# Kernel optimization log

Measured on AMD Instinct MI355X. Metric: run time of the kernel, lower is better.

## Reference

```python
import jax, jax.numpy as jnp
import numpy as np
from jax import lax

# Inference-mode (training=False) ROIGenerator constants
PRE_NMS_TOPK = 1000
POST_NMS_TOPK = 1000
IOU_THRESHOLD = 0.7
SCORE_THRESHOLD = 0.0

LEVEL_SIZES = {2: 196608, 3: 49152, 4: 12288, 5: 3072}
BATCH = 8


def _make_boxes(key, shape):
    # valid yxyx boxes: y1 < y2, x1 < x2
    k1, k2 = jax.random.split(key)
    yx = jax.random.uniform(k1, shape[:-1] + (2,), dtype=jnp.float32) * 1000.0
    hw = jax.random.uniform(k2, shape[:-1] + (2,), dtype=jnp.float32) * 100.0 + 1.0
    return jnp.concatenate([yx, yx + hw], axis=-1)  # [B, N, 4] yxyx


def setup_inputs() -> dict:
    key = jax.random.key(0)
    ks = jax.random.split(key, 8)
    inp = {}
    for i, lvl in enumerate(sorted(LEVEL_SIZES)):
        n = LEVEL_SIZES[lvl]
        inp[f"boxes_p{lvl}"] = _make_boxes(ks[2 * i], (BATCH, n, 4))
        inp[f"scores_p{lvl}"] = jax.random.normal(ks[2 * i + 1], (BATCH, n), dtype=jnp.float32)
    return inp


def _pairwise_iou(b):
    # b: [B, K, 4] in yxyx -> iou: [B, K, K]
    y1, x1, y2, x2 = jnp.split(b, 4, axis=-1)           # each [B, K, 1]
    area = ((y2 - y1) * (x2 - x1))[..., 0]              # [B, K]
    iy1 = jnp.maximum(y1, jnp.swapaxes(y1, 1, 2))
    ix1 = jnp.maximum(x1, jnp.swapaxes(x1, 1, 2))
    iy2 = jnp.minimum(y2, jnp.swapaxes(y2, 1, 2))
    ix2 = jnp.minimum(x2, jnp.swapaxes(x2, 1, 2))
    ih = jnp.clip(iy2 - iy1, 0.0)
    iw = jnp.clip(ix2 - ix1, 0.0)
    inter = ih * iw                                     # [B, K, K]
    union = area[:, :, None] + area[:, None, :] - inter
    return jnp.where(union > 0, inter / union, 0.0)


def _per_level_gen(boxes, scores):
    # boxes: [B, N, 4] yxyx, scores: [B, N]
    n = scores.shape[1]
    pre_k = min(n, PRE_NMS_TOPK)
    post_k = min(n, POST_NMS_TOPK)

    s, idx = lax.top_k(scores, pre_k)                    # sorted desc, [B, pre_k]
    b = jnp.take_along_axis(boxes, idx[..., None], axis=1)  # [B, pre_k, 4]

    suppress = _pairwise_iou(b) > IOU_THRESHOLD          # [B, pre_k, pre_k]
    keep0 = s > SCORE_THRESHOLD                          # score filter
    ar = jnp.arange(pre_k)

    def step(i, keep):
        # box i suppressed if any earlier kept box overlaps it
        sup_i = jnp.any(suppress[:, :, i] & keep & (ar < i)[None, :], axis=1)
        return keep.at[:, i].set(keep[:, i] & ~sup_i)

    keep = lax.fori_loop(0, pre_k, step, keep0)          # [B, pre_k]

    # kept indices first (stable -> preserves score order), padded selection
    order = jnp.argsort((~keep).astype(jnp.int32), axis=1)  # jax argsort is stable
    sel = order[:, :post_k]                              # [B, post_k]
    num_valid = keep.sum(axis=1)                         # [B]

    level_rois = jnp.take_along_axis(b, sel[..., None], axis=1)   # [B, post_k, 4]
    level_scores = jnp.take_along_axis(s, sel, axis=1)            # [B, post_k]
    vmask = jnp.arange(post_k)[None, :] < num_valid[:, None]      # zero out padding
    level_rois = level_rois * vmask[..., None].astype(level_rois.dtype)
    level_scores = level_scores * vmask.astype(level_scores.dtype)
    return level_rois, level_scores


def _roi_generator(boxes_p2, boxes_p3, boxes_p4, boxes_p5,
                   scores_p2, scores_p3, scores_p4, scores_p5):
    levels = [(boxes_p2, scores_p2), (boxes_p3, scores_p3),
              (boxes_p4, scores_p4), (boxes_p5, scores_p5)]
    rois, roi_scores = [], []
    for b, s in levels:
        r, rs = _per_level_gen(b, s)
        rois.append(r)
        roi_scores.append(rs)
    rois = jnp.concatenate(rois, axis=1)                 # [B, 4*post_k, 4]
    roi_scores = jnp.concatenate(roi_scores, axis=1)     # [B, 4*post_k]
    overall_k = min(roi_scores.shape[1], POST_NMS_TOPK)
    roi_scores, sorted_idx = lax.top_k(roi_scores, overall_k)
    rois = jnp.take_along_axis(rois, sorted_idx[..., None], axis=1)
    return rois, roi_scores


def reference(boxes_p2, boxes_p3, boxes_p4, boxes_p5,
              scores_p2, scores_p3, scores_p4, scores_p5):
    return _roi_generator(boxes_p2, boxes_p3, boxes_p4, boxes_p5,
                          scores_p2, scores_p3, scores_p4, scores_p5)
```

## Files before the change

kernel.cpp:

```cpp
#include <hip/hip_runtime.h>

#define PRE_K 1000
#define CAP   2048
#define NBIN  8192
#define NB    1000
#define NW    16
#define TOT   4000
#define NLVL  4
#define BATCH 8
#define HB    8
#define MBM   16

__device__ __forceinline__ unsigned f2key(float f) {
    unsigned u = __float_as_uint(f);
    return (u & 0x80000000u) ? ~u : (u | 0x80000000u);
}
__device__ __forceinline__ float key2f(unsigned k) {
    unsigned u = (k & 0x80000000u) ? (k & 0x7FFFFFFFu) : ~k;
    return __uint_as_float(u);
}
__device__ __forceinline__ const float* lvl_scores(
    const float* s0, const float* s1, const float* s2, const float* s3, int lvl) {
    switch (lvl) { case 0: return s0; case 1: return s1; case 2: return s2; default: return s3; }
}
__device__ __forceinline__ const float* lvl_boxes(
    const float* b0, const float* b1, const float* b2, const float* b3, int lvl) {
    switch (lvl) { case 0: return b0; case 1: return b1; case 2: return b2; default: return b3; }
}
__device__ __forceinline__ int lvl_n(int lvl) {
    const int sizes[4] = {196608, 49152, 12288, 3072};
    return sizes[lvl];
}
__device__ __forceinline__ float bcast_f(float v, int i) {
    return __int_as_float(__builtin_amdgcn_readlane(__float_as_int(v), i));
}

__global__ __launch_bounds__(512) void hist_kernel(
    const float* __restrict__ scores0, const float* __restrict__ scores1,
    const float* __restrict__ scores2, const float* __restrict__ scores3,
    unsigned* __restrict__ ghist,
    unsigned* __restrict__ counters,
    unsigned long long* __restrict__ ws_nz)
{
    const int blk = blockIdx.x / HB;
    const int hb  = blockIdx.x % HB;
    const int b   = blk >> 2;
    const int lvl = blk & 3;
    const int n   = lvl_n(lvl);
    const float* sc = lvl_scores(scores0, scores1, scores2, scores3, lvl) + (size_t)b * n;

    __shared__ unsigned lhist[2][NBIN];
    const int tid = threadIdx.x;
    const int rep = (tid >> 6) & 1;
    for (int i = tid; i < 2 * NBIN; i += 512) (&lhist[0][0])[i] = 0u;
    if (hb == 0) {
        if (tid == 0) counters[blk] = 0u;
        if (tid < NW) ws_nz[(size_t)blk * NW + tid] = 0ull;
    }
    __syncthreads();

    const float4* sc4 = (const float4*)sc;
    const int n4 = n >> 2;
    for (int i = hb * 512 + tid; i < n4; i += HB * 512) {
        float4 v = sc4[i];
        atomicAdd(&lhist[rep][f2key(v.x) >> 19], 1u);
        atomicAdd(&lhist[rep][f2key(v.y) >> 19], 1u);
        atomicAdd(&lhist[rep][f2key(v.z) >> 19], 1u);
        atomicAdd(&lhist[rep][f2key(v.w) >> 19], 1u);
    }
    __syncthreads();

    unsigned* gh = ghist + ((size_t)blk * HB + hb) * NBIN;
    for (int i = tid; i < NBIN; i += 512)
        gh[i] = lhist[0][i] + lhist[1][i];
}

__global__ __launch_bounds__(512) void collect_kernel(
    const float* __restrict__ scores0, const float* __restrict__ scores1,
    const float* __restrict__ scores2, const float* __restrict__ scores3,
    const unsigned* __restrict__ ghist,
    unsigned* __restrict__ counters,
    unsigned long long* __restrict__ cand)
{
    const int blk = blockIdx.x / HB;
    const int hb  = blockIdx.x % HB;
    const int b   = blk >> 2;
    const int lvl = blk & 3;
    const int n   = lvl_n(lvl);
    const float* sc = lvl_scores(scores0, scores1, scores2, scores3, lvl) + (size_t)b * n;
    unsigned long long* candp = cand + (size_t)blk * CAP;

    __shared__ unsigned hsum[NBIN];
    __shared__ unsigned csum[256];
    __shared__ int s_chunk;
    __shared__ unsigned s_before, sT;
    __shared__ unsigned long long cbuf[CAP];
    __shared__ unsigned ccnt, cbase;

    const int tid  = threadIdx.x;
    const int lane = tid & 63;
    if (tid == 0) ccnt = 0;

    for (int i = tid; i < NBIN; i += 512) {
        unsigned v = 0;
        #pragma unroll
        for (int p = 0; p < HB; ++p)
            v += ghist[((size_t)blk * HB + p) * NBIN + i];
        hsum[i] = v;
    }
    __syncthreads();
    if (tid < 256) {
        unsigned s = 0;
        #pragma unroll
        for (int k = 0; k < 32; ++k)
            s += hsum[tid * 32 + ((k + tid) & 31)];
        csum[tid] = s;
    }
    __syncthreads();
    if (tid < 256) {
        unsigned suf = 0;
        for (int c = tid + 1; c < 256; ++c) suf += csum[c];
        if (suf < PRE_K && suf + csum[tid] >= PRE_K) { s_chunk = tid; s_before = suf; }
    }
    __syncthreads();
    if (tid == 0) {
        int C = s_chunk;
        unsigned acc = s_before;
        int T = C * 32;
        for (int bin = C * 32 + 31; bin >= C * 32; --bin) {
            acc += hsum[bin];
            if (acc >= PRE_K) { T = bin; break; }
        }
        sT = (unsigned)T;
    }
    __syncthreads();
    const unsigned T = sT;

    for (int i = hb * 512 + tid; i < n; i += HB * 512) {
        unsigned key = f2key(sc[i]);
        bool pred = (key >> 19) >= T;
        unsigned long long act = __ballot(pred);
        if (act) {
            int leader = __ffsll((long long)act) - 1;
            unsigned base = 0;
            if (lane == leader) base = atomicAdd(&ccnt, (unsigned)__popcll(act));
            base = __shfl(base, leader, 64);
            if (pred) {
                unsigned pos = base + (unsigned)__popcll(act & ((1ull << lane) - 1ull));
                if (pos < CAP)
                    cbuf[pos] = ((unsigned long long)key << 32) | (unsigned)(~i);
            }
        }
    }
    __syncthreads();
    unsigned cnt = ccnt; if (cnt > CAP) cnt = CAP;
    if (tid == 0) cbase = atomicAdd(&counters[blk], cnt);
    __syncthreads();
    const unsigned gb = cbase;
    for (unsigned i = tid; i < cnt; i += 512) {
        unsigned p = gb + i;
        if (p < CAP) candp[p] = cbuf[i];
    }
}

__global__ __launch_bounds__(1024) void sortemit_kernel(
    const float* __restrict__ boxes0, const float* __restrict__ boxes1,
    const float* __restrict__ boxes2, const float* __restrict__ boxes3,
    const unsigned* __restrict__ counters,
    const unsigned long long* __restrict__ cand,
    float* __restrict__ ws_scores,
    float* __restrict__ ws_boxes)
{
    const int blk = blockIdx.x;
    const int b   = blk >> 2;
    const int lvl = blk & 3;
    const int n   = lvl_n(lvl);
    const float* bx = lvl_boxes(boxes0, boxes1, boxes2, boxes3, lvl) + (size_t)b * n * 4;
    const unsigned long long* candp = cand + (size_t)blk * CAP;

    __shared__ unsigned long long arr[CAP];
    const int tid = threadIdx.x;
    unsigned cnt = counters[blk]; if (cnt > CAP) cnt = CAP;

    for (int i = tid; i < CAP; i += 1024)
        arr[i] = (i < (int)cnt) ? candp[i] : 0ull;
    __syncthreads();

    for (unsigned kk = 2; kk <= CAP; kk <<= 1) {
        for (unsigned j = kk >> 1; j > 0; j >>= 1) {
            for (unsigned i = tid; i < CAP; i += 1024) {
                unsigned p = i ^ j;
                if (p > i) {
                    unsigned long long a = arr[i], c = arr[p];
                    bool desc = ((i & kk) == 0);
                    if (desc ? (a < c) : (a > c)) { arr[i] = c; arr[p] = a; }
                }
            }
            __syncthreads();
        }
    }

    for (int r = tid; r < PRE_K; r += 1024) {
        unsigned long long c = arr[r];
        unsigned key = (unsigned)(c >> 32);
        int idx = (int)(~(unsigned)c);
        ws_scores[(size_t)blk * PRE_K + r] = key2f(key);
        float* dst = ws_boxes + ((size_t)blk * PRE_K + r) * 4;
        const float* src = bx + (size_t)idx * 4;
        dst[0] = src[0]; dst[1] = src[1]; dst[2] = src[2]; dst[3] = src[3];
    }
}

__global__ __launch_bounds__(256) void mask_kernel(
    const float* __restrict__ ws_boxes,
    unsigned long long* __restrict__ ws_mask,
    unsigned long long* __restrict__ ws_nz)
{
    const int blk  = blockIdx.x / MBM;
    const int mb   = blockIdx.x % MBM;
    const int tid  = threadIdx.x;
    const int lane = tid & 63;
    const int wv   = tid >> 6;

    __shared__ float4 sbox[1024];

    const float4* bxp = (const float4*)(ws_boxes + (size_t)blk * NB * 4);
    for (int i = tid; i < 1024; i += 256)
        sbox[i] = (i < NB) ? bxp[i] : make_float4(0.f, 0.f, 0.f, 0.f);
    __syncthreads();

    unsigned long long* maskp = ws_mask + (size_t)blk * NB * NW;
    unsigned long long* nzp   = ws_nz + (size_t)blk * NW;
    const double CSUM = (double)__uint_as_float(0x3F333333u)
                      + (double)__uint_as_float(0x3F333334u);

    for (int t = mb * 4 + wv; t < 136; t += MBM * 4) {
        int w = 0, acc = 0;
        while (acc + w + 1 <= t) { acc += w + 1; ++w; }
        const int rb = t - acc;
        const int rbase = rb * 64;

        const float4 rbx = sbox[rbase + lane];
        const float   ra = (rbx.z - rbx.x) * (rbx.w - rbx.y);
        const float4 cbx = sbox[w * 64 + lane];
        const float   ca = (cbx.z - cbx.x) * (cbx.w - cbx.y);

        unsigned long long myw = 0ull;
        #pragma unroll
        for (int jj = 0; jj < 64; ++jj) {
            const float cy1 = bcast_f(cbx.x, jj);
            const float cx1 = bcast_f(cbx.y, jj);
            const float cy2 = bcast_f(cbx.z, jj);
            const float cx2 = bcast_f(cbx.w, jj);
            const float caj = bcast_f(ca, jj);
            float iy1 = fmaxf(rbx.x, cy1);
            float ix1 = fmaxf(rbx.y, cx1);
            float iy2 = fminf(rbx.z, cy2);
            float ix2 = fminf(rbx.w, cx2);
            float ih = fmaxf(iy2 - iy1, 0.0f);
            float iw = fmaxf(ix2 - ix1, 0.0f);
            float inter = ih * iw;
            float uni = ra + caj - inter;
            bool pred = (uni > 0.0f) &&
                        (2.0 * (double)inter >= CSUM * (double)uni);
            myw |= ((unsigned long long)pred) << jj;
        }
        if (w == rb)
            myw &= ~((2ull << lane) - 1ull);
        if (rbase + lane < NB)
            maskp[(size_t)(rbase + lane) * NW + w] = myw;
        unsigned long long nzb = __ballot(myw != 0ull);
        if (lane == 0 && nzb) atomicOr(&nzp[rb], nzb);
    }
}

__global__ __launch_bounds__(1024) void greedy_kernel(
    float* __restrict__ ws_scores,
    float* __restrict__ ws_boxes,
    const unsigned long long* __restrict__ ws_mask,
    const unsigned long long* __restrict__ ws_nz)
{
    const int blk  = blockIdx.x;
    const int tid  = threadIdx.x;
    const int lane = tid & 63;
    const int wv   = tid >> 6;

    __shared__ unsigned long long Mrow[NB * NW];
    __shared__ float4 sbox[NB];
    __shared__ float  ssc[NB];
    __shared__ unsigned long long nzlds[NW];
    __shared__ unsigned long long keepw[NW];
    __shared__ int wprefix[NW];
    __shared__ int slist[NB];
    __shared__ int sL;

    float* scp = ws_scores + (size_t)blk * NB;
    float* bxp = ws_boxes  + (size_t)blk * NB * 4;
    const unsigned long long* mrows = ws_mask + (size_t)blk * NB * NW;

    if (tid < NW) nzlds[tid] = ws_nz[(size_t)blk * NW + tid];
    for (int i = tid; i < NB; i += 1024) {
        sbox[i] = ((const float4*)bxp)[i];
        ssc[i]  = scp[i];
    }
    {
        const int j = wv * 64 + lane;
        bool pred = (j < NB) && (scp[j] > 0.0f);
        unsigned long long bal = __ballot(pred);
        if (lane == 0) keepw[wv] = bal;
    }
    __syncthreads();

    if (tid == 0) {
        int L = 0;
        for (int c = 0; c < NW; ++c) {
            unsigned long long p = nzlds[c];
            while (p) {
                int i = __ffsll((long long)p) - 1;
                slist[L++] = c * 64 + i;
                p &= p - 1;
            }
        }
        sL = L;
    }
    __syncthreads();
    const int L = sL;

    for (int idx = tid; idx < L * NW; idx += 1024) {
        int r = slist[idx >> 4];
        Mrow[idx] = mrows[(size_t)r * NW + (idx & 15)];
    }
    __syncthreads();

    if (tid < 64) {
        unsigned long long kp = (lane < NW) ? keepw[lane] : 0ull;
        unsigned long long mnext = (L > 0 && lane < NW) ? Mrow[lane] : 0ull;
        int rnext = (L > 0) ? slist[0] : 0;
        for (int k = 0; k < L; ++k) {
            unsigned long long m = mnext;
            const int r = rnext;
            if (k + 1 < L) {
                rnext = slist[k + 1];
                mnext = (lane < NW) ? Mrow[(size_t)(k + 1) * NW + lane] : 0ull;
            }
            const int c = r >> 6;
            unsigned klo = (unsigned)__builtin_amdgcn_readlane((int)(unsigned)kp, c);
            unsigned khi = (unsigned)__builtin_amdgcn_readlane((int)(unsigned)(kp >> 32), c);
            unsigned long long kw = ((unsigned long long)khi << 32) | klo;
            if ((kw >> (r & 63)) & 1ull) {
                unsigned long long mm = (lane >= c) ? m : 0ull;
                kp &= ~mm;
            }
        }
        if (lane < NW) keepw[lane] = kp;
    }
    __syncthreads();
    if (tid == 0) {
        int acc = 0;
        for (int w = 0; w < NW; ++w) { wprefix[w] = acc; acc += __popcll(keepw[w]); }
    }
    __syncthreads();

    for (int i = tid; i < NB; i += 1024) scp[i] = 0.0f;
    for (int i = tid; i < NB * 4; i += 1024) bxp[i] = 0.0f;
    __syncthreads();
    for (int i = tid; i < NB; i += 1024) {
        const int w = i >> 6;
        const unsigned long long kw = keepw[w];
        if ((kw >> (i & 63)) & 1ull) {
            int rank = wprefix[w] + __popcll(kw & ((1ull << (i & 63)) - 1ull));
            scp[rank] = ssc[i];
            float4 bb = sbox[i];
            float* dst = bxp + (size_t)rank * 4;
            dst[0] = bb.x; dst[1] = bb.y; dst[2] = bb.z; dst[3] = bb.w;
        }
    }
}

__global__ __launch_bounds__(1024) void final_merge_kernel(
    const float* __restrict__ ws_scores,
    const float* __restrict__ ws_boxes,
    float* __restrict__ out)
{
    const int blk = blockIdx.x;
    const int b   = blk >> 2;
    const int lvl = blk & 3;
    const int tid = threadIdx.x;

    __shared__ unsigned long long lists[NLVL][PRE_K];

    for (int i = tid; i < TOT; i += 1024) {
        unsigned u = f2key(ws_scores[(size_t)b * TOT + i]);
        lists[i / PRE_K][i % PRE_K] =
            ((unsigned long long)u << 32) | (unsigned)(~i);
    }
    __syncthreads();

    float* out_rois   = out;
    float* out_scores = out + 32000;

    for (int r = tid; r < PRE_K; r += 1024) {
        const unsigned long long c = lists[lvl][r];
        int rank = r;
        #pragma unroll
        for (int l = 0; l < NLVL; ++l) {
            if (l == lvl) continue;
            int lo = 0, hi = PRE_K;
            while (lo < hi) {
                int mid = (lo + hi) >> 1;
                if (lists[l][mid] > c) lo = mid + 1; else hi = mid;
            }
            rank += lo;
        }
        if (rank < PRE_K) {
            out_scores[(size_t)b * PRE_K + rank] = key2f((unsigned)(c >> 32));
            const int pos = lvl * PRE_K + r;
            const float4 bb = ((const float4*)ws_boxes)[(size_t)b * TOT + pos];
            float* dst = out_rois + ((size_t)b * PRE_K + rank) * 4;
            dst[0] = bb.x; dst[1] = bb.y; dst[2] = bb.z; dst[3] = bb.w;
        }
    }
}

extern "C" void kernel_launch(void* const* d_in, const int* in_sizes, int n_in,
                              void* d_out, int out_size, void* d_ws, size_t ws_size,
                              hipStream_t stream) {
    const float* boxes0  = (const float*)d_in[0];
    const float* scores0 = (const float*)d_in[1];
    const float* boxes1  = (const float*)d_in[2];
    const float* scores1 = (const float*)d_in[3];
    const float* boxes2  = (const float*)d_in[4];
    const float* scores2 = (const float*)d_in[5];
    const float* boxes3  = (const float*)d_in[6];
    const float* scores3 = (const float*)d_in[7];
    float* out = (float*)d_out;

    char* base = (char*)d_ws;
    float* ws_scores = (float*)base;
    float* ws_boxes  = (float*)(base + 128000);
    unsigned long long* ws_mask = (unsigned long long*)(base + 640000);
    unsigned long long* ws_nz   = (unsigned long long*)(base + 4736000);
    unsigned long long* cand    = (unsigned long long*)(base + 4740096);
    unsigned* ghist             = (unsigned*)(base + 5264384);
    unsigned* counters          = (unsigned*)(base + 13652992);

    hist_kernel<<<BATCH * NLVL * HB, 512, 0, stream>>>(
        scores0, scores1, scores2, scores3, ghist, counters, ws_nz);
    collect_kernel<<<BATCH * NLVL * HB, 512, 0, stream>>>(
        scores0, scores1, scores2, scores3, ghist, counters, cand);
    sortemit_kernel<<<BATCH * NLVL, 1024, 0, stream>>>(
        boxes0, boxes1, boxes2, boxes3, counters, cand, ws_scores, ws_boxes);
    mask_kernel<<<BATCH * NLVL * MBM, 256, 0, stream>>>(ws_boxes, ws_mask, ws_nz);
    greedy_kernel<<<BATCH * NLVL, 1024, 0, stream>>>(ws_scores, ws_boxes, ws_mask, ws_nz);
    final_merge_kernel<<<BATCH * NLVL, 1024, 0, stream>>>(ws_scores, ws_boxes, out);
}
```

Before: 114.6 us.

## Fuse histogram, collect, sort, mask and greedy NMS into one per-level kernel

Replaces five kernels (histogram, candidate collect, bitonic sort, IoU mask, greedy NMS) with one kernel per (batch, level) block of 1024 threads. A single shared buffer is reused for the 4-replica histogram, the candidate list and the XOR-swizzled IoU mask, so the mask and candidates never go through global memory. This removes launch overhead and global round-trips. In exchange the histogram and collect passes now run on only 32 blocks instead of 256, which lowers parallelism for the large P2 level (196k scores read twice by one block).

```diff
diff --git a/kernel.cpp b/kernel.cpp
--- a/kernel.cpp
+++ b/kernel.cpp
@@ -3,13 +3,12 @@
 #define PRE_K 1000
 #define CAP   2048
 #define NBIN  8192
+#define NREP  4
 #define NB    1000
 #define NW    16
 #define TOT   4000
 #define NLVL  4
 #define BATCH 8
-#define HB    8
-#define MBM   16
 
 __device__ __forceinline__ unsigned f2key(float f) {
     unsigned u = __float_as_uint(f);
@@ -35,139 +34,11 @@
     return __int_as_float(__builtin_amdgcn_readlane(__float_as_int(v), i));
 }
 
-__global__ __launch_bounds__(512) void hist_kernel(
-    const float* __restrict__ scores0, const float* __restrict__ scores1,
-    const float* __restrict__ scores2, const float* __restrict__ scores3,
-    unsigned* __restrict__ ghist,
-    unsigned* __restrict__ counters,
-    unsigned long long* __restrict__ ws_nz)
-{
-    const int blk = blockIdx.x / HB;
-    const int hb  = blockIdx.x % HB;
-    const int b   = blk >> 2;
-    const int lvl = blk & 3;
-    const int n   = lvl_n(lvl);
-    const float* sc = lvl_scores(scores0, scores1, scores2, scores3, lvl) + (size_t)b * n;
-
-    __shared__ unsigned lhist[2][NBIN];
-    const int tid = threadIdx.x;
-    const int rep = (tid >> 6) & 1;
-    for (int i = tid; i < 2 * NBIN; i += 512) (&lhist[0][0])[i] = 0u;
-    if (hb == 0) {
-        if (tid == 0) counters[blk] = 0u;
-        if (tid < NW) ws_nz[(size_t)blk * NW + tid] = 0ull;
-    }
-    __syncthreads();
-
-    const float4* sc4 = (const float4*)sc;
-    const int n4 = n >> 2;
-    for (int i = hb * 512 + tid; i < n4; i += HB * 512) {
-        float4 v = sc4[i];
-        atomicAdd(&lhist[rep][f2key(v.x) >> 19], 1u);
-        atomicAdd(&lhist[rep][f2key(v.y) >> 19], 1u);
-        atomicAdd(&lhist[rep][f2key(v.z) >> 19], 1u);
-        atomicAdd(&lhist[rep][f2key(v.w) >> 19], 1u);
-    }
-    __syncthreads();
-
-    unsigned* gh = ghist + ((size_t)blk * HB + hb) * NBIN;
-    for (int i = tid; i < NBIN; i += 512)
-        gh[i] = lhist[0][i] + lhist[1][i];
-}
-
-__global__ __launch_bounds__(512) void collect_kernel(
-    const float* __restrict__ scores0, const float* __restrict__ scores1,
-    const float* __restrict__ scores2, const float* __restrict__ scores3,
-    const unsigned* __restrict__ ghist,
-    unsigned* __restrict__ counters,
-    unsigned long long* __restrict__ cand)
-{
-    const int blk = blockIdx.x / HB;
-    const int hb  = blockIdx.x % HB;
-    const int b   = blk >> 2;
-    const int lvl = blk & 3;
-    const int n   = lvl_n(lvl);
-    const float* sc = lvl_scores(scores0, scores1, scores2, scores3, lvl) + (size_t)b * n;
-    unsigned long long* candp = cand + (size_t)blk * CAP;
-
-    __shared__ unsigned hsum[NBIN];
-    __shared__ unsigned csum[256];
-    __shared__ int s_chunk;
-    __shared__ unsigned s_before, sT;
-    __shared__ unsigned long long cbuf[CAP];
-    __shared__ unsigned ccnt, cbase;
-
-    const int tid  = threadIdx.x;
-    const int lane = tid & 63;
-    if (tid == 0) ccnt = 0;
-
-    for (int i = tid; i < NBIN; i += 512) {
-        unsigned v = 0;
-        #pragma unroll
-        for (int p = 0; p < HB; ++p)
-            v += ghist[((size_t)blk * HB + p) * NBIN + i];
-        hsum[i] = v;
-    }
-    __syncthreads();
-    if (tid < 256) {
-        unsigned s = 0;
-        #pragma unroll
-        for (int k = 0; k < 32; ++k)
-            s += hsum[tid * 32 + ((k + tid) & 31)];
-        csum[tid] = s;
-    }
-    __syncthreads();
-    if (tid < 256) {
-        unsigned suf = 0;
-        for (int c = tid + 1; c < 256; ++c) suf += csum[c];
-        if (suf < PRE_K && suf + csum[tid] >= PRE_K) { s_chunk = tid; s_before = suf; }
-    }
-    __syncthreads();
-    if (tid == 0) {
-        int C = s_chunk;
-        unsigned acc = s_before;
-        int T = C * 32;
-        for (int bin = C * 32 + 31; bin >= C * 32; --bin) {
-            acc += hsum[bin];
-            if (acc >= PRE_K) { T = bin; break; }
-        }
-        sT = (unsigned)T;
-    }
-    __syncthreads();
-    const unsigned T = sT;
-
-    for (int i = hb * 512 + tid; i < n; i += HB * 512) {
-        unsigned key = f2key(sc[i]);
-        bool pred = (key >> 19) >= T;
-        unsigned long long act = __ballot(pred);
-        if (act) {
-            int leader = __ffsll((long long)act) - 1;
-            unsigned base = 0;
-            if (lane == leader) base = atomicAdd(&ccnt, (unsigned)__popcll(act));
-            base = __shfl(base, leader, 64);
-            if (pred) {
-                unsigned pos = base + (unsigned)__popcll(act & ((1ull << lane) - 1ull));
-                if (pos < CAP)
-                    cbuf[pos] = ((unsigned long long)key << 32) | (unsigned)(~i);
-            }
-        }
-    }
-    __syncthreads();
-    unsigned cnt = ccnt; if (cnt > CAP) cnt = CAP;
-    if (tid == 0) cbase = atomicAdd(&counters[blk], cnt);
-    __syncthreads();
-    const unsigned gb = cbase;
-    for (unsigned i = tid; i < cnt; i += 512) {
-        unsigned p = gb + i;
-        if (p < CAP) candp[p] = cbuf[i];
-    }
-}
-
-__global__ __launch_bounds__(1024) void sortemit_kernel(
-    const float* __restrict__ boxes0, const float* __restrict__ boxes1,
-    const float* __restrict__ boxes2, const float* __restrict__ boxes3,
-    const unsigned* __restrict__ counters,
-    const unsigned long long* __restrict__ cand,
+__global__ __launch_bounds__(1024) void fused_level_kernel(
+    const float* __restrict__ boxes0, const float* __restrict__ scores0,
+    const float* __restrict__ boxes1, const float* __restrict__ scores1,
+    const float* __restrict__ boxes2, const float* __restrict__ scores2,
+    const float* __restrict__ boxes3, const float* __restrict__ scores3,
     float* __restrict__ ws_scores,
     float* __restrict__ ws_boxes)
 {
@@ -175,15 +46,105 @@
     const int b   = blk >> 2;
     const int lvl = blk & 3;
     const int n   = lvl_n(lvl);
+    const float* sc = lvl_scores(scores0, scores1, scores2, scores3, lvl) + (size_t)b * n;
     const float* bx = lvl_boxes(boxes0, boxes1, boxes2, boxes3, lvl) + (size_t)b * n * 4;
-    const unsigned long long* candp = cand + (size_t)blk * CAP;
-
-    __shared__ unsigned long long arr[CAP];
-    const int tid = threadIdx.x;
-    unsigned cnt = counters[blk]; if (cnt > CAP) cnt = CAP;
-
-    for (int i = tid; i < CAP; i += 1024)
-        arr[i] = (i < (int)cnt) ? candp[i] : 0ull;
+
+    __shared__ __align__(16) unsigned long long A[1024 * NW];
+    __shared__ float4 sbox[1024];
+    __shared__ float  ssc[1024];
+    __shared__ int    slist[NB];
+    __shared__ unsigned csum[256];
+    __shared__ unsigned long long nzlds[NW], keepw[NW];
+    __shared__ int wprefix[NW];
+    __shared__ unsigned s_chunk, s_before, sT, ccnt;
+    __shared__ int sL;
+
+    const int tid  = threadIdx.x;
+    const int lane = tid & 63;
+    const int wv   = tid >> 6;
+
+    unsigned* lhist = (unsigned*)A;
+    for (int i = tid; i < NREP * NBIN; i += 1024) lhist[i] = 0u;
+    if (tid < NW) nzlds[tid] = 0ull;
+    if (tid == 0) ccnt = 0u;
+    __syncthreads();
+    {
+        const unsigned roff = (unsigned)(wv & (NREP - 1)) * NBIN;
+        const float4* sc4 = (const float4*)sc;
+        const int n4 = n >> 2;
+        for (int i = tid; i < n4; i += 1024) {
+            float4 v = sc4[i];
+            atomicAdd(&lhist[roff + (f2key(v.x) >> 19)], 1u);
+            atomicAdd(&lhist[roff + (f2key(v.y) >> 19)], 1u);
+            atomicAdd(&lhist[roff + (f2key(v.z) >> 19)], 1u);
+            atomicAdd(&lhist[roff + (f2key(v.w) >> 19)], 1u);
+        }
+    }
+    __syncthreads();
+
+    if (tid < 256) {
+        unsigned s = 0;
+        #pragma unroll 8
+        for (int k = 0; k < 32; ++k) {
+            int bin = tid * 32 + ((k + tid) & 31);
+            s += lhist[bin] + lhist[NBIN + bin] + lhist[2*NBIN + bin] + lhist[3*NBIN + bin];
+        }
+        csum[tid] = s;
+    }
+    __syncthreads();
+    if (tid < 256) {
+        unsigned suf = 0;
+        for (int c = tid + 1; c < 256; ++c) suf += csum[c];
+        if (suf < PRE_K && suf + csum[tid] >= PRE_K) { s_chunk = tid; s_before = suf; }
+    }
+    __syncthreads();
+    if (tid == 0) {
+        int C = (int)s_chunk;
+        unsigned acc = s_before;
+        int T = C * 32;
+        for (int bin = C * 32 + 31; bin >= C * 32; --bin) {
+            acc += lhist[bin] + lhist[NBIN + bin] + lhist[2*NBIN + bin] + lhist[3*NBIN + bin];
+            if (acc >= PRE_K) { T = bin; break; }
+        }
+        sT = (unsigned)T;
+    }
+    __syncthreads();
+    const unsigned T = sT;
+    __syncthreads();
+
+    unsigned long long* cbuf = A;
+    {
+        const float4* sc4 = (const float4*)sc;
+        const int n4 = n >> 2;
+        for (int i = tid; i < n4; i += 1024) {
+            float4 v = sc4[i];
+            #pragma unroll
+            for (int c4 = 0; c4 < 4; ++c4) {
+                float f = (c4 == 0) ? v.x : (c4 == 1) ? v.y : (c4 == 2) ? v.z : v.w;
+                unsigned key = f2key(f);
+                bool pred = (key >> 19) >= T;
+                unsigned long long act = __ballot(pred);
+                if (act) {
+                    int leader = __ffsll((long long)act) - 1;
+                    unsigned base = 0;
+                    if (lane == leader) base = atomicAdd(&ccnt, (unsigned)__popcll(act));
+                    base = __shfl(base, leader, 64);
+                    if (pred) {
+                        unsigned pos = base + (unsigned)__popcll(act & ((1ull << lane) - 1ull));
+                        int idx = i * 4 + c4;
+                        if (pos < CAP)
+                            cbuf[pos] = ((unsigned long long)key << 32) | (unsigned)(~idx);
+                    }
+                }
+            }
+        }
+    }
+    __syncthreads();
+    {
+        unsigned cnt = ccnt; if (cnt > CAP) cnt = CAP;
+        for (int i = tid; i < CAP; i += 1024)
+            if (i >= (int)cnt) cbuf[i] = 0ull;
+    }
     __syncthreads();
 
     for (unsigned kk = 2; kk <= CAP; kk <<= 1) {
@@ -191,50 +152,31 @@
             for (unsigned i = tid; i < CAP; i += 1024) {
                 unsigned p = i ^ j;
                 if (p > i) {
-                    unsigned long long a = arr[i], c = arr[p];
+                    unsigned long long a = cbuf[i], c = cbuf[p];
                     bool desc = ((i & kk) == 0);
-                    if (desc ? (a < c) : (a > c)) { arr[i] = c; arr[p] = a; }
+                    if (desc ? (a < c) : (a > c)) { cbuf[i] = c; cbuf[p] = a; }
                 }
             }
             __syncthreads();
         }
     }
 
-    for (int r = tid; r < PRE_K; r += 1024) {
-        unsigned long long c = arr[r];
-        unsigned key = (unsigned)(c >> 32);
-        int idx = (int)(~(unsigned)c);
-        ws_scores[(size_t)blk * PRE_K + r] = key2f(key);
-        float* dst = ws_boxes + ((size_t)blk * PRE_K + r) * 4;
-        const float* src = bx + (size_t)idx * 4;
-        dst[0] = src[0]; dst[1] = src[1]; dst[2] = src[2]; dst[3] = src[3];
-    }
-}
-
-__global__ __launch_bounds__(256) void mask_kernel(
-    const float* __restrict__ ws_boxes,
-    unsigned long long* __restrict__ ws_mask,
-    unsigned long long* __restrict__ ws_nz)
-{
-    const int blk  = blockIdx.x / MBM;
-    const int mb   = blockIdx.x % MBM;
-    const int tid  = threadIdx.x;
-    const int lane = tid & 63;
-    const int wv   = tid >> 6;
-
-    __shared__ float4 sbox[1024];
-
-    const float4* bxp = (const float4*)(ws_boxes + (size_t)blk * NB * 4);
-    for (int i = tid; i < 1024; i += 256)
-        sbox[i] = (i < NB) ? bxp[i] : make_float4(0.f, 0.f, 0.f, 0.f);
-    __syncthreads();
-
-    unsigned long long* maskp = ws_mask + (size_t)blk * NB * NW;
-    unsigned long long* nzp   = ws_nz + (size_t)blk * NW;
-    const double CSUM = (double)__uint_as_float(0x3F333333u)
-                      + (double)__uint_as_float(0x3F333334u);
-
-    for (int t = mb * 4 + wv; t < 136; t += MBM * 4) {
+    {
+        const int r = tid;
+        if (r < PRE_K) {
+            unsigned long long c = cbuf[r];
+            int idx = (int)(~(unsigned)c);
+            sbox[r] = ((const float4*)bx)[idx];
+            ssc[r]  = key2f((unsigned)(c >> 32));
+        } else {
+            sbox[r] = make_float4(0.f, 0.f, 0.f, 0.f);
+            ssc[r]  = 0.f;
+        }
+    }
+    __syncthreads();
+
+    unsigned long long* Mlds = A;
+    for (int t = wv; t < 136; t += 16) {
         int w = 0, acc = 0;
         while (acc + w + 1 <= t) { acc += w + 1; ++w; }
         const int rb = t - acc;
@@ -244,6 +186,8 @@
         const float   ra = (rbx.z - rbx.x) * (rbx.w - rbx.y);
         const float4 cbx = sbox[w * 64 + lane];
         const float   ca = (cbx.z - cbx.x) * (cbx.w - cbx.y);
+        const double CSUM = (double)__uint_as_float(0x3F333333u)
+                          + (double)__uint_as_float(0x3F333334u);
 
         unsigned long long myw = 0ull;
         #pragma unroll
@@ -267,45 +211,14 @@
         }
         if (w == rb)
             myw &= ~((2ull << lane) - 1ull);
-        if (rbase + lane < NB)
-            maskp[(size_t)(rbase + lane) * NW + w] = myw;
+        const int row = rbase + lane;
+        Mlds[row * NW + (w ^ (lane & 15))] = myw;
         unsigned long long nzb = __ballot(myw != 0ull);
-        if (lane == 0 && nzb) atomicOr(&nzp[rb], nzb);
-    }
-}
-
-__global__ __launch_bounds__(1024) void greedy_kernel(
-    float* __restrict__ ws_scores,
-    float* __restrict__ ws_boxes,
-    const unsigned long long* __restrict__ ws_mask,
-    const unsigned long long* __restrict__ ws_nz)
-{
-    const int blk  = blockIdx.x;
-    const int tid  = threadIdx.x;
-    const int lane = tid & 63;
-    const int wv   = tid >> 6;
-
-    __shared__ unsigned long long Mrow[NB * NW];
-    __shared__ float4 sbox[NB];
-    __shared__ float  ssc[NB];
-    __shared__ unsigned long long nzlds[NW];
-    __shared__ unsigned long long keepw[NW];
-    __shared__ int wprefix[NW];
-    __shared__ int slist[NB];
-    __shared__ int sL;
-
-    float* scp = ws_scores + (size_t)blk * NB;
-    float* bxp = ws_boxes  + (size_t)blk * NB * 4;
-    const unsigned long long* mrows = ws_mask + (size_t)blk * NB * NW;
-
-    if (tid < NW) nzlds[tid] = ws_nz[(size_t)blk * NW + tid];
-    for (int i = tid; i < NB; i += 1024) {
-        sbox[i] = ((const float4*)bxp)[i];
-        ssc[i]  = scp[i];
+        if (lane == 0 && nzb) atomicOr(&nzlds[rb], nzb);
     }
     {
         const int j = wv * 64 + lane;
-        bool pred = (j < NB) && (scp[j] > 0.0f);
+        bool pred = (j < NB) && (ssc[j] > 0.0f);
         unsigned long long bal = __ballot(pred);
         if (lane == 0) keepw[wv] = bal;
     }
@@ -325,23 +238,17 @@
     }
     __syncthreads();
     const int L = sL;
-
-    for (int idx = tid; idx < L * NW; idx += 1024) {
-        int r = slist[idx >> 4];
-        Mrow[idx] = mrows[(size_t)r * NW + (idx & 15)];
-    }
-    __syncthreads();
-
     if (tid < 64) {
         unsigned long long kp = (lane < NW) ? keepw[lane] : 0ull;
-        unsigned long long mnext = (L > 0 && lane < NW) ? Mrow[lane] : 0ull;
         int rnext = (L > 0) ? slist[0] : 0;
+        unsigned long long mnext = (L > 0 && lane < NW)
+            ? Mlds[rnext * NW + (lane ^ (rnext & 15))] : 0ull;
         for (int k = 0; k < L; ++k) {
             unsigned long long m = mnext;
             const int r = rnext;
             if (k + 1 < L) {
                 rnext = slist[k + 1];
-                mnext = (lane < NW) ? Mrow[(size_t)(k + 1) * NW + lane] : 0ull;
+                mnext = (lane < NW) ? Mlds[rnext * NW + (lane ^ (rnext & 15))] : 0ull;
             }
             const int c = r >> 6;
             unsigned klo = (unsigned)__builtin_amdgcn_readlane((int)(unsigned)kp, c);
@@ -361,6 +268,8 @@
     }
     __syncthreads();
 
+    float* scp = ws_scores + (size_t)blk * NB;
+    float* bxp = ws_boxes  + (size_t)blk * NB * 4;
     for (int i = tid; i < NB; i += 1024) scp[i] = 0.0f;
     for (int i = tid; i < NB * 4; i += 1024) bxp[i] = 0.0f;
     __syncthreads();
@@ -435,22 +344,11 @@
     const float* scores3 = (const float*)d_in[7];
     float* out = (float*)d_out;
 
-    char* base = (char*)d_ws;
-    float* ws_scores = (float*)base;
-    float* ws_boxes  = (float*)(base + 128000);
-    unsigned long long* ws_mask = (unsigned long long*)(base + 640000);
-    unsigned long long* ws_nz   = (unsigned long long*)(base + 4736000);
-    unsigned long long* cand    = (unsigned long long*)(base + 4740096);
-    unsigned* ghist             = (unsigned*)(base + 5264384);
-    unsigned* counters          = (unsigned*)(base + 13652992);
-
-    hist_kernel<<<BATCH * NLVL * HB, 512, 0, stream>>>(
-        scores0, scores1, scores2, scores3, ghist, counters, ws_nz);
-    collect_kernel<<<BATCH * NLVL * HB, 512, 0, stream>>>(
-        scores0, scores1, scores2, scores3, ghist, counters, cand);
-    sortemit_kernel<<<BATCH * NLVL, 1024, 0, stream>>>(
-        boxes0, boxes1, boxes2, boxes3, counters, cand, ws_scores, ws_boxes);
-    mask_kernel<<<BATCH * NLVL * MBM, 256, 0, stream>>>(ws_boxes, ws_mask, ws_nz);
-    greedy_kernel<<<BATCH * NLVL, 1024, 0, stream>>>(ws_scores, ws_boxes, ws_mask, ws_nz);
+    float* ws_scores = (float*)d_ws;
+    float* ws_boxes  = ws_scores + 32 * PRE_K;
+
+    fused_level_kernel<<<BATCH * NLVL, 1024, 0, stream>>>(
+        boxes0, scores0, boxes1, scores1, boxes2, scores2, boxes3, scores3,
+        ws_scores, ws_boxes);
     final_merge_kernel<<<BATCH * NLVL, 1024, 0, stream>>>(ws_scores, ws_boxes, out);
 }
```

Result: slower. 212.6 us (+85.5%).
